# Performance work log

Hardware: AMD Instinct MI355X
Metric: run time of the kernel (lower is better)

Reference implementation:

```python
import jax, jax.numpy as jnp
import numpy as np

N = 100000; E = 1600000; D_IN = 9; HID = 16; HEADS = 8; D = HID * HEADS; G = 1000
NEG_SLOPE = 0.2; LN_EPS = 1e-5


def _gat_conv(x, src, dst, W, a_src, a_dst, b, heads, ch):
    # PyG GATConv (eval mode, self-loops already appended to src/dst)
    h = (x @ W).reshape(-1, heads, ch)                   # [N,H,C]
    al_s = (h * a_src).sum(-1)                           # [N,H]
    al_d = (h * a_dst).sum(-1)                           # [N,H]
    e = al_s[src] + al_d[dst]                            # [Et,H]
    e = jnp.where(e > 0, e, NEG_SLOPE * e)               # LeakyReLU(0.2)
    m = jax.ops.segment_max(e, dst, num_segments=N)      # per-dst softmax
    alpha = jnp.exp(e - m[dst])
    denom = jax.ops.segment_sum(alpha, dst, num_segments=N)
    alpha = alpha / (denom[dst] + 1e-16)
    out = jax.ops.segment_sum(h[src] * alpha[:, :, None], dst, num_segments=N)
    return out.reshape(-1, heads * ch) + b


def _ln_graph(x, g, b):
    # PyG LayerNorm, mode='graph', batch=None: normalize over all nodes+channels
    mu = x.mean()
    var = jnp.mean((x - mu) ** 2)
    return (x - mu) / jnp.sqrt(var + LN_EPS) * g + b


def setup_inputs() -> dict:
    key = jax.random.key(0)
    ks = jax.random.split(key, 20)
    s = 0.1
    p = lambda i, shape: jax.random.normal(ks[i], shape, jnp.float32) * s
    return {
        "x": jax.random.normal(ks[0], (N, D_IN), jnp.float32),
        "edge_index": jax.random.randint(ks[1], (2, E), 0, N),
        "batch": jnp.sort(jax.random.randint(ks[2], (N,), 0, G)),
        "W1": p(3, (D_IN, D)), "a_src1": p(4, (HEADS, HID)), "a_dst1": p(5, (HEADS, HID)), "b1": jnp.zeros((D,), jnp.float32),
        "W2": p(6, (D, D)), "a_src2": p(7, (1, D)), "a_dst2": p(8, (1, D)), "b2": jnp.zeros((D,), jnp.float32),
        "fc1_w": p(9, (D, D)), "fc1_b": jnp.zeros((D,), jnp.float32),
        "fc2_w": p(10, (D, D)), "fc2_b": jnp.zeros((D,), jnp.float32),
        "fc3_w": p(11, (D, D)), "fc3_b": jnp.zeros((D,), jnp.float32),
        "fc4_w": p(12, (D, D)), "fc4_b": jnp.zeros((D,), jnp.float32),
        "g1": jnp.ones((D,), jnp.float32), "beta1": jnp.zeros((D,), jnp.float32),
        "g2": jnp.ones((D,), jnp.float32), "beta2": jnp.zeros((D,), jnp.float32),
        "fcf_w": p(13, (D, 1)), "fcf_b": jnp.zeros((1,), jnp.float32),
    }


def reference(x, edge_index, batch, W1, a_src1, a_dst1, b1, W2, a_src2, a_dst2, b2,
              fc1_w, fc1_b, fc2_w, fc2_b, fc3_w, fc3_b, fc4_w, fc4_b,
              g1, beta1, g2, beta2, fcf_w, fcf_b):
    loops = jnp.arange(N)
    src = jnp.concatenate([edge_index[0], loops])
    dst = jnp.concatenate([edge_index[1], loops])
    h = jax.nn.relu(_gat_conv(x, src, dst, W1, a_src1, a_dst1, b1, HEADS, HID))
    hc = h
    h = jax.nn.relu(h @ fc1_w + fc1_b)
    h = jax.nn.relu(h @ fc2_w + fc2_b + hc)
    h = _ln_graph(h, g1, beta1)
    hc = h
    h = _gat_conv(h, src, dst, W2, a_src2, a_dst2, b2, 1, D)
    h = jax.nn.relu(h @ fc3_w + fc3_b)
    h = h @ fc4_w + fc4_b + hc
    h = _ln_graph(h, g2, beta2)
    h = h @ fcf_w + fcf_b                                # [N,1]
    sums = jax.ops.segment_sum(h, batch, num_segments=G)
    cnt = jax.ops.segment_sum(jnp.ones((N,), h.dtype), batch, num_segments=G)
    return sums / jnp.maximum(cnt, 1.0)[:, None]          # global_mean_pool -> [G,1]
```

## Files before the change

kernel.cpp:

```cpp
#include <hip/hip_runtime.h>
#include <cstdint>

#define NN 100000
#define NE 1600000
#define DI 9
#define DD 128
#define NH 8
#define NG 1000

#define NBK 3125
#define NBLK 256
#define EPB (NE/NBLK)

typedef unsigned int uint;
typedef __attribute__((ext_vector_type(8))) short bf16x8;
typedef __attribute__((ext_vector_type(4))) float f32x4;

__device__ __forceinline__ float leaky(float x){ return x > 0.f ? x : 0.2f*x; }
__device__ __forceinline__ uint f2bf(float f){
  uint u = __float_as_uint(f);
  return (u + 0x7fffu + ((u>>16)&1u)) >> 16;
}
__device__ __forceinline__ float bflo(uint p){ return __uint_as_float(p << 16); }
__device__ __forceinline__ float bfhi(uint p){ return __uint_as_float(p & 0xffff0000u); }
__device__ __forceinline__ uint packbf(float a, float b){ return f2bf(a) | (f2bf(b)<<16); }

union U16 { uint4 u; bf16x8 v; };
__device__ __forceinline__ bf16x8 ld8(const uint* p){ U16 t; t.u = *(const uint4*)p; return t.v; }

__global__ __launch_bounds__(512) void k_hist(const int* __restrict__ dst, int* __restrict__ hist){
  __shared__ int h[NBK];
  for (int i = threadIdx.x; i < NBK; i += 512) h[i] = 0;
  __syncthreads();
  int blk = blockIdx.x;
  int beg = blk*EPB, end = beg + EPB;
  for (int i = beg + threadIdx.x; i < end; i += 512)
    atomicAdd(&h[dst[i] >> 5], 1);
  __syncthreads();
  for (int b = threadIdx.x; b < NBK; b += 512) hist[(size_t)blk*NBK + b] = h[b];
}

__global__ __launch_bounds__(256) void k_bsum(int* __restrict__ hist, int* __restrict__ bsum){
  int b = blockIdx.x*256 + threadIdx.x;
  if (b >= NBK) return;
  int run = 0;
  for (int k = 0; k < NBLK; ++k){
    int t = hist[(size_t)k*NBK + b];
    hist[(size_t)k*NBK + b] = run;
    run += t;
  }
  bsum[b] = run;
}

__global__ __launch_bounds__(1024) void k_bscan(const int* __restrict__ bsum, int* __restrict__ bbase){
  __shared__ int sh[1024];
  __shared__ int carry;
  if (threadIdx.x == 0) carry = 0;
  __syncthreads();
  for (int c0 = 0; c0 < NBK; c0 += 1024){
    int i = c0 + threadIdx.x;
    int v = (i < NBK) ? bsum[i] : 0;
    sh[threadIdx.x] = v;
    __syncthreads();
    for (int off = 1; off < 1024; off <<= 1){
      int t = (threadIdx.x >= off) ? sh[threadIdx.x-off] : 0;
      __syncthreads();
      sh[threadIdx.x] += t;
      __syncthreads();
    }
    if (i < NBK) bbase[i] = carry + sh[threadIdx.x] - v;
    __syncthreads();
    if (threadIdx.x == 0) carry += sh[1023];
    __syncthreads();
  }
}

__global__ __launch_bounds__(512) void k_part(const int* __restrict__ src, const int* __restrict__ dst,
    const int* __restrict__ hist, const int* __restrict__ bbase, uint* __restrict__ ebuf){
  __shared__ int cur[NBK];
  int blk = blockIdx.x;
  for (int b = threadIdx.x; b < NBK; b += 512)
    cur[b] = hist[(size_t)blk*NBK + b] + bbase[b];
  __syncthreads();
  int beg = blk*EPB, end = beg + EPB;
  for (int i = beg + threadIdx.x; i < end; i += 512){
    int d = dst[i], s = src[i];
    int b = d >> 5;
    int p = atomicAdd(&cur[b], 1);
    ebuf[p] = (uint)s | ((uint)(d & 31) << 26);
  }
}

__global__ __launch_bounds__(64) void k_fin(const uint* __restrict__ ebuf, const int* __restrict__ bbase,
    const int* __restrict__ bsum, int* __restrict__ rowptr, int* __restrict__ col){
  __shared__ int cnt32[32];
  __shared__ int exc[32];
  int b = blockIdx.x;
  int lane = threadIdx.x;
  if (lane < 32) cnt32[lane] = 0;
  __syncthreads();
  int base = bbase[b], n = bsum[b];
  for (int i = lane; i < n; i += 64)
    atomicAdd(&cnt32[ebuf[base+i] >> 26], 1);
  __syncthreads();
  if (lane == 0){
    int run = 0;
    for (int d = 0; d < 32; ++d){
      int t = cnt32[d];
      exc[d] = run;
      rowptr[b*32 + d] = base + run;
      run += t;
    }
  }
  __syncthreads();
  if (lane < 32) cnt32[lane] = exc[lane];
  __syncthreads();
  for (int i = lane; i < n; i += 64){
    uint e = ebuf[base+i];
    int d = e >> 26;
    int r = atomicAdd(&cnt32[d], 1);
    col[base + r] = (int)(e & 0x03ffffffu);
  }
  if (b == 0 && lane == 0) rowptr[NN] = NE;
}

__global__ __launch_bounds__(64) void k_wconv(const float* __restrict__ W, uint* __restrict__ WT){
  int n = blockIdx.x;
  int t = threadIdx.x;
  float w0 = W[(2*t)*DD + n];
  float w1 = W[(2*t+1)*DD + n];
  WT[n*64 + t] = packbf(w0, w1);
}

__global__ __launch_bounds__(128) void k_lin1(const float* __restrict__ x, const float* __restrict__ W1,
    const float* __restrict__ as1, const float* __restrict__ ad1,
    uint* __restrict__ t1b, float* __restrict__ al_s, float* __restrict__ al_d){
  int n = blockIdx.x;
  int c = threadIdx.x;
  const float* xr = x + n*DI;
  float t = 0.f;
  #pragma unroll
  for (int k = 0; k < DI; ++k) t = fmaf(xr[k], W1[k*DD+c], t);
  uint mybf = f2bf(t);
  uint pbf  = (uint)__shfl_xor((int)mybf, 1, 64);
  if (!(c & 1)) t1b[(size_t)n*64 + (c>>1)] = mybf | (pbf<<16);
  float vs = t * as1[c];
  float vd = t * ad1[c];
  #pragma unroll
  for (int m = 8; m >= 1; m >>= 1){ vs += __shfl_xor(vs, m, 16); vd += __shfl_xor(vd, m, 16); }
  if ((c & 15) == 0){
    al_s[n*NH + (c>>4)] = vs;
    al_d[n*NH + (c>>4)] = vd;
  }
}

__global__ __launch_bounds__(256) void k_attn1(const float* __restrict__ al_s, const float* __restrict__ al_d,
    const int* __restrict__ rowptr, const int* __restrict__ col,
    float* __restrict__ alpha, float* __restrict__ a0n, float* __restrict__ invden){
  int n = blockIdx.x*4 + (threadIdx.x >> 6);
  if (n >= NN) return;
  int lane = threadIdx.x & 63;
  int h = lane & 7, j = lane >> 3;
  int beg = rowptr[n], end = rowptr[n+1];
  float ald = al_d[n*NH + h];
  float es = leaky(al_s[n*NH + h] + ald);
  float vmax = -3.4e38f;
  for (int e = beg + j; e < end; e += 8){
    int s = col[e];
    vmax = fmaxf(vmax, leaky(al_s[s*NH + h] + ald));
  }
  vmax = fmaxf(vmax, __shfl_xor(vmax, 8, 64));
  vmax = fmaxf(vmax, __shfl_xor(vmax, 16, 64));
  vmax = fmaxf(vmax, __shfl_xor(vmax, 32, 64));
  float m = fmaxf(es, vmax);
  float sl = 0.f;
  for (int e = beg + j; e < end; e += 8){
    int s = col[e];
    float a = __expf(leaky(al_s[s*NH + h] + ald) - m);
    alpha[(size_t)e*NH + h] = a;
    sl += a;
  }
  sl += __shfl_xor(sl, 8, 64);
  sl += __shfl_xor(sl, 16, 64);
  sl += __shfl_xor(sl, 32, 64);
  float a0 = __expf(es - m);
  float inv = 1.f/(a0 + sl + 1e-16f);
  if (j == 0){
    a0n[n*NH + h]    = a0*inv;
    invden[n*NH + h] = inv;
  }
}

__global__ __launch_bounds__(256) void k_gat1g(const uint* __restrict__ t1b,
    const float* __restrict__ alpha, const float* __restrict__ a0n, const float* __restrict__ invden,
    const int* __restrict__ rowptr, const int* __restrict__ col,
    const float* __restrict__ b1, uint* __restrict__ outb){
  int n = blockIdx.x*4 + (threadIdx.x >> 6);
  if (n >= NN) return;
  int lane = threadIdx.x & 63;
  int h = lane >> 3;
  int beg = rowptr[n], end = rowptr[n+1];
  float s0 = 0.f, s1 = 0.f;
  int e = beg;
  for (; e + 4 <= end; e += 4){
    int c0 = col[e], c1 = col[e+1], c2 = col[e+2], c3 = col[e+3];
    float a0_ = alpha[(size_t)e*NH + h];
    float a1_ = alpha[(size_t)(e+1)*NH + h];
    float a2_ = alpha[(size_t)(e+2)*NH + h];
    float a3_ = alpha[(size_t)(e+3)*NH + h];
    uint p0 = t1b[(size_t)c0*64 + lane];
    uint p1 = t1b[(size_t)c1*64 + lane];
    uint p2 = t1b[(size_t)c2*64 + lane];
    uint p3 = t1b[(size_t)c3*64 + lane];
    s0 = fmaf(a0_, bflo(p0), s0); s1 = fmaf(a0_, bfhi(p0), s1);
    s0 = fmaf(a1_, bflo(p1), s0); s1 = fmaf(a1_, bfhi(p1), s1);
    s0 = fmaf(a2_, bflo(p2), s0); s1 = fmaf(a2_, bfhi(p2), s1);
    s0 = fmaf(a3_, bflo(p3), s0); s1 = fmaf(a3_, bfhi(p3), s1);
  }
  for (; e < end; ++e){
    float a = alpha[(size_t)e*NH + h];
    uint p = t1b[(size_t)col[e]*64 + lane];
    s0 = fmaf(a, bflo(p), s0); s1 = fmaf(a, bfhi(p), s1);
  }
  uint ps = t1b[(size_t)n*64 + lane];
  float inv = invden[n*NH + h], az = a0n[n*NH + h];
  float2 bb = ((const float2*)b1)[lane];
  float r0 = fmaf(inv, s0, az*bflo(ps)) + bb.x;
  float r1 = fmaf(inv, s1, az*bfhi(ps)) + bb.y;
  outb[(size_t)n*64 + lane] = packbf(fmaxf(r0,0.f), fmaxf(r1,0.f));
}

__global__ __launch_bounds__(256) void k_al2(const uint* __restrict__ t2b,
    const float* __restrict__ as2, const float* __restrict__ ad2,
    float* __restrict__ al_s, float* __restrict__ al_d){
  int n = blockIdx.x*4 + (threadIdx.x >> 6);
  if (n >= NN) return;
  int lane = threadIdx.x & 63;
  uint p = t2b[(size_t)n*64 + lane];
  float v0 = bflo(p), v1 = bfhi(p);
  float2 s2 = ((const float2*)as2)[lane];
  float2 d2 = ((const float2*)ad2)[lane];
  float vs = v0*s2.x + v1*s2.y;
  float vd = v0*d2.x + v1*d2.y;
  #pragma unroll
  for (int m = 32; m >= 1; m >>= 1){ vs += __shfl_xor(vs, m, 64); vd += __shfl_xor(vd, m, 64); }
  if (lane == 0){ al_s[n] = vs; al_d[n] = vd; }
}

__global__ __launch_bounds__(256) void k_attn2(const float* __restrict__ al_s, const float* __restrict__ al_d,
    const int* __restrict__ rowptr, const int* __restrict__ col,
    float* __restrict__ alpha, float* __restrict__ a0n, float* __restrict__ invden){
  int n = blockIdx.x*4 + (threadIdx.x >> 6);
  if (n >= NN) return;
  int lane = threadIdx.x & 63;
  int beg = rowptr[n], end = rowptr[n+1];
  float ald = al_d[n];
  float es = leaky(al_s[n] + ald);
  float vmax = -3.4e38f;
  for (int e = beg + lane; e < end; e += 64)
    vmax = fmaxf(vmax, leaky(al_s[col[e]] + ald));
  #pragma unroll
  for (int mk = 32; mk >= 1; mk >>= 1) vmax = fmaxf(vmax, __shfl_xor(vmax, mk, 64));
  float m = fmaxf(es, vmax);
  float sl = 0.f;
  for (int e = beg + lane; e < end; e += 64){
    float a = __expf(leaky(al_s[col[e]] + ald) - m);
    alpha[e] = a;
    sl += a;
  }
  #pragma unroll
  for (int mk = 32; mk >= 1; mk >>= 1) sl += __shfl_xor(sl, mk, 64);
  float a0 = __expf(es - m);
  float inv = 1.f/(a0 + sl + 1e-16f);
  if (lane == 0){ a0n[n] = a0*inv; invden[n] = inv; }
}

__global__ __launch_bounds__(256) void k_gat2g(const uint* __restrict__ t2b,
    const float* __restrict__ alpha, const float* __restrict__ a0n, const float* __restrict__ invden,
    const int* __restrict__ rowptr, const int* __restrict__ col,
    const float* __restrict__ b2, uint* __restrict__ outb){
  int n = blockIdx.x*4 + (threadIdx.x >> 6);
  if (n >= NN) return;
  int lane = threadIdx.x & 63;
  int beg = rowptr[n], end = rowptr[n+1];
  float s0 = 0.f, s1 = 0.f;
  int e = beg;
  for (; e + 4 <= end; e += 4){
    int c0 = col[e], c1 = col[e+1], c2 = col[e+2], c3 = col[e+3];
    float a0_ = alpha[e],   a1_ = alpha[e+1];
    float a2_ = alpha[e+2], a3_ = alpha[e+3];
    uint p0 = t2b[(size_t)c0*64 + lane];
    uint p1 = t2b[(size_t)c1*64 + lane];
    uint p2 = t2b[(size_t)c2*64 + lane];
    uint p3 = t2b[(size_t)c3*64 + lane];
    s0 = fmaf(a0_, bflo(p0), s0); s1 = fmaf(a0_, bfhi(p0), s1);
    s0 = fmaf(a1_, bflo(p1), s0); s1 = fmaf(a1_, bfhi(p1), s1);
    s0 = fmaf(a2_, bflo(p2), s0); s1 = fmaf(a2_, bfhi(p2), s1);
    s0 = fmaf(a3_, bflo(p3), s0); s1 = fmaf(a3_, bfhi(p3), s1);
  }
  for (; e < end; ++e){
    float a = alpha[e];
    uint p = t2b[(size_t)col[e]*64 + lane];
    s0 = fmaf(a, bflo(p), s0); s1 = fmaf(a, bfhi(p), s1);
  }
  uint ps = t2b[(size_t)n*64 + lane];
  float inv = invden[n], az = a0n[n];
  float2 bb = ((const float2*)b2)[lane];
  float r0 = fmaf(inv, s0, az*bflo(ps)) + bb.x;
  float r1 = fmaf(inv, s1, az*bfhi(ps)) + bb.y;
  outb[(size_t)n*64 + lane] = packbf(r0, r1);
}

template<bool RELU, bool BIAS, bool RES>
__global__ __launch_bounds__(256) void k_mfma(const uint* __restrict__ Xb, const uint* __restrict__ WTb,
    const float* __restrict__ bias, const uint* __restrict__ resb, uint* __restrict__ outb, int nrows){
  int lane = threadIdx.x & 63;
  int wid  = threadIdx.x >> 6;
  int m0 = blockIdx.x*128 + wid*32;
  int lr = lane & 15, hi4 = lane >> 4;
  f32x4 acc[2][8];
  #pragma unroll
  for (int a = 0; a < 2; ++a)
    #pragma unroll
    for (int c = 0; c < 8; ++c) acc[a][c] = (f32x4){0.f,0.f,0.f,0.f};
  int ra0 = m0 + lr;      if (ra0 > NN-1) ra0 = NN-1;
  int ra1 = m0 + 16 + lr; if (ra1 > NN-1) ra1 = NN-1;
  #pragma unroll
  for (int kk = 0; kk < 4; ++kk){
    int ko = kk*16 + hi4*4;
    bf16x8 a0 = ld8(Xb + (size_t)ra0*64 + ko);
    bf16x8 a1 = ld8(Xb + (size_t)ra1*64 + ko);
    #pragma unroll
    for (int c = 0; c < 8; ++c){
      bf16x8 b = ld8(WTb + (size_t)(c*16 + lr)*64 + ko);
      acc[0][c] = __builtin_amdgcn_mfma_f32_16x16x32_bf16(a0, b, acc[0][c], 0, 0, 0);
      acc[1][c] = __builtin_amdgcn_mfma_f32_16x16x32_bf16(a1, b, acc[1][c], 0, 0, 0);
    }
  }
  bool evn = !(lane & 1);
  int cph = lr >> 1;
  #pragma unroll
  for (int rg = 0; rg < 2; ++rg){
    #pragma unroll
    for (int c = 0; c < 8; ++c){
      int cp = c*8 + cph;
      #pragma unroll
      for (int r = 0; r < 4; ++r){
        float v0 = acc[rg][c][r];
        float v1 = __shfl_xor(v0, 1, 64);
        int row = m0 + rg*16 + hi4*4 + r;
        if (evn && row < nrows){
          if (BIAS){ float2 bb = ((const float2*)bias)[cp]; v0 += bb.x; v1 += bb.y; }
          if (RES){ uint rr = resb[(size_t)row*64 + cp]; v0 += bflo(rr); v1 += bfhi(rr); }
          if (RELU){ v0 = fmaxf(v0, 0.f); v1 = fmaxf(v1, 0.f); }
          outb[(size_t)row*64 + cp] = packbf(v0, v1);
        }
      }
    }
  }
}

__global__ __launch_bounds__(256) void k_ln_reduce_bf(const uint* __restrict__ xb, float* __restrict__ pbuf){
  const uint4* x4 = (const uint4*)xb;
  const int n4 = NN*16;
  float s = 0.f, ss = 0.f;
  for (int i = blockIdx.x*256 + threadIdx.x; i < n4; i += gridDim.x*256){
    uint4 u = x4[i];
    float a, b;
    a = bflo(u.x); b = bfhi(u.x); s += a+b; ss += a*a + b*b;
    a = bflo(u.y); b = bfhi(u.y); s += a+b; ss += a*a + b*b;
    a = bflo(u.z); b = bfhi(u.z); s += a+b; ss += a*a + b*b;
    a = bflo(u.w); b = bfhi(u.w); s += a+b; ss += a*a + b*b;
  }
  #pragma unroll
  for (int m = 32; m >= 1; m >>= 1){ s += __shfl_xor(s, m, 64); ss += __shfl_xor(ss, m, 64); }
  __shared__ float sh[8];
  int wid = threadIdx.x >> 6, lane = threadIdx.x & 63;
  if (lane == 0){ sh[wid*2] = s; sh[wid*2+1] = ss; }
  __syncthreads();
  if (threadIdx.x == 0){
    float S = 0.f, SS = 0.f;
    for (int w = 0; w < 4; ++w){ S += sh[2*w]; SS += sh[2*w+1]; }
    pbuf[blockIdx.x*2] = S; pbuf[blockIdx.x*2+1] = SS;
  }
}

__global__ __launch_bounds__(256) void k_ln_stats(const float* __restrict__ pbuf, float* __restrict__ stats, int nb){
  float s = 0.f, ss = 0.f;
  for (int i = threadIdx.x; i < nb; i += 256){ s += pbuf[2*i]; ss += pbuf[2*i+1]; }
  #pragma unroll
  for (int m = 32; m >= 1; m >>= 1){ s += __shfl_xor(s, m, 64); ss += __shfl_xor(ss, m, 64); }
  __shared__ float sh[8];
  int wid = threadIdx.x >> 6, lane = threadIdx.x & 63;
  if (lane == 0){ sh[wid*2] = s; sh[wid*2+1] = ss; }
  __syncthreads();
  if (threadIdx.x == 0){
    float S = 0.f, SS = 0.f;
    for (int w = 0; w < 4; ++w){ S += sh[2*w]; SS += sh[2*w+1]; }
    const float inv = 1.f/((float)NN*(float)DD);
    float mu = S*inv;
    float var = SS*inv - mu*mu;
    stats[0] = mu;
    stats[1] = rsqrtf(var + 1e-5f);
  }
}

__global__ __launch_bounds__(256) void k_ln_apply_bf(uint* __restrict__ xb, const float* __restrict__ g,
    const float* __restrict__ be, const float* __restrict__ stats){
  const int n4 = NN*16;
  float mu = stats[0], rs = stats[1];
  uint4* x4 = (uint4*)xb;
  const float2* g2 = (const float2*)g;
  const float2* b2 = (const float2*)be;
  for (int i = blockIdx.x*256 + threadIdx.x; i < n4; i += gridDim.x*256){
    int cb = (i & 15)*4;
    uint4 u = x4[i];
    float2 ga = g2[cb],   gb = g2[cb+1], gc = g2[cb+2], gd = g2[cb+3];
    float2 ba = b2[cb],   bb = b2[cb+1], bc = b2[cb+2], bd = b2[cb+3];
    u.x = packbf((bflo(u.x)-mu)*rs*ga.x + ba.x, (bfhi(u.x)-mu)*rs*ga.y + ba.y);
    u.y = packbf((bflo(u.y)-mu)*rs*gb.x + bb.x, (bfhi(u.y)-mu)*rs*gb.y + bb.y);
    u.z = packbf((bflo(u.z)-mu)*rs*gc.x + bc.x, (bfhi(u.z)-mu)*rs*gc.y + bc.y);
    u.w = packbf((bflo(u.w)-mu)*rs*gd.x + bd.x, (bfhi(u.w)-mu)*rs*gd.y + bd.y);
    x4[i] = u;
  }
}

__global__ __launch_bounds__(256) void k_fdot_ln(const uint* __restrict__ xb, const float* __restrict__ g,
    const float* __restrict__ be, const float* __restrict__ stats,
    const float* __restrict__ fw, const float* __restrict__ fb, float* __restrict__ val){
  int n = blockIdx.x*4 + (threadIdx.x >> 6);
  if (n >= NN) return;
  int lane = threadIdx.x & 63;
  float mu = stats[0], rs = stats[1];
  uint p = xb[(size_t)n*64 + lane];
  float2 gg = ((const float2*)g)[lane];
  float2 bb = ((const float2*)be)[lane];
  float2 ww = ((const float2*)fw)[lane];
  float v = ((bflo(p)-mu)*rs*gg.x + bb.x)*ww.x + ((bfhi(p)-mu)*rs*gg.y + bb.y)*ww.y;
  #pragma unroll
  for (int m = 32; m >= 1; m >>= 1) v += __shfl_xor(v, m, 64);
  if (lane == 0) val[n] = v + fb[0];
}

__global__ __launch_bounds__(64) void k_pool(const float* __restrict__ val, const int* __restrict__ batch,
                                             float* __restrict__ out){
  int g = blockIdx.x;
  int lane = threadIdx.x;
  int lo = 0, hi = NN;
  while (lo < hi){ int mid = (lo+hi)>>1; if (batch[mid] < g) lo = mid+1; else hi = mid; }
  int start = lo;
  hi = NN;
  while (lo < hi){ int mid = (lo+hi)>>1; if (batch[mid] < g+1) lo = mid+1; else hi = mid; }
  int end = lo;
  float s = 0.f;
  for (int i = start + lane; i < end; i += 64) s += val[i];
  #pragma unroll
  for (int m = 32; m >= 1; m >>= 1) s += __shfl_xor(s, m, 64);
  if (lane == 0) out[g] = s / fmaxf((float)(end - start), 1.f);
}

extern "C" void kernel_launch(void* const* d_in, const int* in_sizes, int n_in,
                              void* d_out, int out_size, void* d_ws, size_t ws_size,
                              hipStream_t stream){
  const float* x   = (const float*)d_in[0];
  const int*   ei  = (const int*)d_in[1];
  const int* batch = (const int*)d_in[2];
  const float* W1  = (const float*)d_in[3];
  const float* as1 = (const float*)d_in[4];
  const float* ad1 = (const float*)d_in[5];
  const float* b1  = (const float*)d_in[6];
  const float* W2  = (const float*)d_in[7];
  const float* as2 = (const float*)d_in[8];
  const float* ad2 = (const float*)d_in[9];
  const float* b2  = (const float*)d_in[10];
  const float* fc1w= (const float*)d_in[11];
  const float* fc1b= (const float*)d_in[12];
  const float* fc2w= (const float*)d_in[13];
  const float* fc2b= (const float*)d_in[14];
  const float* fc3w= (const float*)d_in[15];
  const float* fc3b= (const float*)d_in[16];
  const float* fc4w= (const float*)d_in[17];
  const float* fc4b= (const float*)d_in[18];
  const float* g1  = (const float*)d_in[19];
  const float* be1 = (const float*)d_in[20];
  const float* g2  = (const float*)d_in[21];
  const float* be2 = (const float*)d_in[22];
  const float* fcw = (const float*)d_in[23];
  const float* fcb = (const float*)d_in[24];
  float* out = (float*)d_out;
  (void)in_sizes; (void)n_in; (void)out_size; (void)ws_size;

  char* ws = (char*)d_ws;
  size_t off = 0;
  auto alloc = [&](size_t bytes)->void*{
    void* p = ws + off;
    off += (bytes + 255) & ~(size_t)255;
    return p;
  };
  float* A    = (float*)alloc((size_t)NN*DD*4);
  float* B    = (float*)alloc((size_t)NN*DD*4);
  float* C    = (float*)alloc((size_t)NN*DD*4);
  float* als1 = (float*)alloc((size_t)NN*NH*4);
  float* ald1 = (float*)alloc((size_t)NN*NH*4);
  float* a0n1 = (float*)alloc((size_t)NN*NH*4);
  float* inv1 = (float*)alloc((size_t)NN*NH*4);
  float* als2 = (float*)alloc((size_t)NN*4);
  float* ald2 = (float*)alloc((size_t)NN*4);
  float* a0n2 = (float*)alloc((size_t)NN*4);
  float* inv2 = (float*)alloc((size_t)NN*4);
  float* alpha2 = (float*)alloc((size_t)NE*4);
  int*   rowptr = (int*)alloc((size_t)(NN+1)*4);
  int*   col    = (int*)alloc((size_t)NE*4);
  int*   bsum   = (int*)alloc((size_t)NBK*4);
  int*   bbase  = (int*)alloc((size_t)NBK*4);
  float* pbuf   = (float*)alloc(1024*2*4);
  float* stats  = (float*)alloc(2*4);
  float* val    = (float*)alloc((size_t)NN*4);
  uint* wt_fc1  = (uint*)alloc((size_t)DD*64*4);
  uint* wt_fc2  = (uint*)alloc((size_t)DD*64*4);
  uint* wt_w2   = (uint*)alloc((size_t)DD*64*4);
  uint* wt_fc3  = (uint*)alloc((size_t)DD*64*4);
  uint* wt_fc4  = (uint*)alloc((size_t)DD*64*4);

  float* alpha1 = C;
  uint*  Ab     = (uint*)A;
  uint*  Bb     = (uint*)B;
  uint*  Cb     = (uint*)C;
  int*   hist   = (int*)A;
  uint*  ebuf   = (uint*)alpha2;

  const int* esrc = ei;
  const int* edst = ei + NE;

  k_hist <<<NBLK, 512, 0, stream>>>(edst, hist);
  k_bsum <<<(NBK+255)/256, 256, 0, stream>>>(hist, bsum);
  k_bscan<<<1, 1024, 0, stream>>>(bsum, bbase);
  k_part <<<NBLK, 512, 0, stream>>>(esrc, edst, hist, bbase, ebuf);
  k_fin  <<<NBK, 64, 0, stream>>>(ebuf, bbase, bsum, rowptr, col);

  k_wconv<<<DD, 64, 0, stream>>>(fc1w, wt_fc1);
  k_wconv<<<DD, 64, 0, stream>>>(fc2w, wt_fc2);
  k_wconv<<<DD, 64, 0, stream>>>(W2,   wt_w2);
  k_wconv<<<DD, 64, 0, stream>>>(fc3w, wt_fc3);
  k_wconv<<<DD, 64, 0, stream>>>(fc4w, wt_fc4);

  const int WB = (NN + 3)/4;
  const int GB = (NN + 127)/128;

  k_lin1<<<NN, 128, 0, stream>>>(x, W1, as1, ad1, Ab, als1, ald1);
  k_attn1<<<WB, 256, 0, stream>>>(als1, ald1, rowptr, col, alpha1, a0n1, inv1);
  k_gat1g<<<WB, 256, 0, stream>>>(Ab, alpha1, a0n1, inv1, rowptr, col, b1, Bb);

  k_mfma<true,  true, false><<<GB, 256, 0, stream>>>(Bb, wt_fc1, fc1b, nullptr, Ab, NN);
  k_mfma<true,  true, true ><<<GB, 256, 0, stream>>>(Ab, wt_fc2, fc2b, Bb,      Cb, NN);

  k_ln_reduce_bf<<<1024, 256, 0, stream>>>(Cb, pbuf);
  k_ln_stats<<<1, 256, 0, stream>>>(pbuf, stats, 1024);
  k_ln_apply_bf<<<1024, 256, 0, stream>>>(Cb, g1, be1, stats);

  k_mfma<false, false, false><<<GB, 256, 0, stream>>>(Cb, wt_w2, nullptr, nullptr, Ab, NN);
  k_al2<<<WB, 256, 0, stream>>>(Ab, as2, ad2, als2, ald2);
  k_attn2<<<WB, 256, 0, stream>>>(als2, ald2, rowptr, col, alpha2, a0n2, inv2);
  k_gat2g<<<WB, 256, 0, stream>>>(Ab, alpha2, a0n2, inv2, rowptr, col, b2, Bb);

  k_mfma<true,  true, false><<<GB, 256, 0, stream>>>(Bb, wt_fc3, fc3b, nullptr, Ab, NN);
  k_mfma<false, true, true ><<<GB, 256, 0, stream>>>(Ab, wt_fc4, fc4b, Cb,      Bb, NN);

  k_ln_reduce_bf<<<1024, 256, 0, stream>>>(Bb, pbuf);
  k_ln_stats<<<1, 256, 0, stream>>>(pbuf, stats, 1024);
  k_fdot_ln<<<WB, 256, 0, stream>>>(Bb, g2, be2, stats, fcw, fcb, val);
  k_pool<<<NG, 64, 0, stream>>>(val, batch, out);
}
```

Baseline: 561.3 us.

## Fuse GAT softmax into aggregation and fold LayerNorm reduction into MFMA epilogue

Removes the separate attention kernels. Each aggregation kernel now computes the unnormalized exp weights on the fly, without max subtraction, and divides by the accumulated denominator at the end. This avoids writing and re-reading the per-edge alpha arrays and launching extra kernels. The LayerNorm sum and sum-of-squares reduction is moved into the epilogue of the residual MFMA GEMM, so the separate full read pass over the activations goes away. Dropping the max subtraction risks overflow in exp for large logits, and the LN statistics are now summed from fp32 values before bf16 rounding.

```diff
diff --git a/kernel.cpp b/kernel.cpp
--- a/kernel.cpp
+++ b/kernel.cpp
@@ -154,80 +154,49 @@
   }
 }
 
-__global__ __launch_bounds__(256) void k_attn1(const float* __restrict__ al_s, const float* __restrict__ al_d,
-    const int* __restrict__ rowptr, const int* __restrict__ col,
-    float* __restrict__ alpha, float* __restrict__ a0n, float* __restrict__ invden){
-  int n = blockIdx.x*4 + (threadIdx.x >> 6);
-  if (n >= NN) return;
-  int lane = threadIdx.x & 63;
-  int h = lane & 7, j = lane >> 3;
-  int beg = rowptr[n], end = rowptr[n+1];
-  float ald = al_d[n*NH + h];
-  float es = leaky(al_s[n*NH + h] + ald);
-  float vmax = -3.4e38f;
-  for (int e = beg + j; e < end; e += 8){
-    int s = col[e];
-    vmax = fmaxf(vmax, leaky(al_s[s*NH + h] + ald));
-  }
-  vmax = fmaxf(vmax, __shfl_xor(vmax, 8, 64));
-  vmax = fmaxf(vmax, __shfl_xor(vmax, 16, 64));
-  vmax = fmaxf(vmax, __shfl_xor(vmax, 32, 64));
-  float m = fmaxf(es, vmax);
-  float sl = 0.f;
-  for (int e = beg + j; e < end; e += 8){
-    int s = col[e];
-    float a = __expf(leaky(al_s[s*NH + h] + ald) - m);
-    alpha[(size_t)e*NH + h] = a;
-    sl += a;
-  }
-  sl += __shfl_xor(sl, 8, 64);
-  sl += __shfl_xor(sl, 16, 64);
-  sl += __shfl_xor(sl, 32, 64);
-  float a0 = __expf(es - m);
-  float inv = 1.f/(a0 + sl + 1e-16f);
-  if (j == 0){
-    a0n[n*NH + h]    = a0*inv;
-    invden[n*NH + h] = inv;
-  }
-}
-
-__global__ __launch_bounds__(256) void k_gat1g(const uint* __restrict__ t1b,
-    const float* __restrict__ alpha, const float* __restrict__ a0n, const float* __restrict__ invden,
+__global__ __launch_bounds__(256) void k_gat1(const uint* __restrict__ t1b,
+    const float* __restrict__ al_s, const float* __restrict__ al_d,
     const int* __restrict__ rowptr, const int* __restrict__ col,
     const float* __restrict__ b1, uint* __restrict__ outb){
   int n = blockIdx.x*4 + (threadIdx.x >> 6);
   if (n >= NN) return;
-  int lane = threadIdx.x & 63;
-  int h = lane >> 3;
+  uint lane = threadIdx.x & 63;
+  uint h = lane >> 3;
+  float ald = al_d[(uint)n*NH + h];
+  float a0  = __expf(leaky(al_s[(uint)n*NH + h] + ald));
+  uint  ps  = t1b[(uint)n*64u + lane];
+  float den = a0;
+  float s0 = a0*bflo(ps), s1 = a0*bfhi(ps);
   int beg = rowptr[n], end = rowptr[n+1];
-  float s0 = 0.f, s1 = 0.f;
   int e = beg;
   for (; e + 4 <= end; e += 4){
-    int c0 = col[e], c1 = col[e+1], c2 = col[e+2], c3 = col[e+3];
-    float a0_ = alpha[(size_t)e*NH + h];
-    float a1_ = alpha[(size_t)(e+1)*NH + h];
-    float a2_ = alpha[(size_t)(e+2)*NH + h];
-    float a3_ = alpha[(size_t)(e+3)*NH + h];
-    uint p0 = t1b[(size_t)c0*64 + lane];
-    uint p1 = t1b[(size_t)c1*64 + lane];
-    uint p2 = t1b[(size_t)c2*64 + lane];
-    uint p3 = t1b[(size_t)c3*64 + lane];
+    uint c0 = (uint)col[e], c1 = (uint)col[e+1], c2 = (uint)col[e+2], c3 = (uint)col[e+3];
+    float l0 = al_s[c0*8u + h], l1 = al_s[c1*8u + h];
+    float l2 = al_s[c2*8u + h], l3 = al_s[c3*8u + h];
+    uint p0 = t1b[c0*64u + lane];
+    uint p1 = t1b[c1*64u + lane];
+    uint p2 = t1b[c2*64u + lane];
+    uint p3 = t1b[c3*64u + lane];
+    float a0_ = __expf(leaky(l0 + ald));
+    float a1_ = __expf(leaky(l1 + ald));
+    float a2_ = __expf(leaky(l2 + ald));
+    float a3_ = __expf(leaky(l3 + ald));
+    den += a0_ + a1_ + a2_ + a3_;
     s0 = fmaf(a0_, bflo(p0), s0); s1 = fmaf(a0_, bfhi(p0), s1);
     s0 = fmaf(a1_, bflo(p1), s0); s1 = fmaf(a1_, bfhi(p1), s1);
     s0 = fmaf(a2_, bflo(p2), s0); s1 = fmaf(a2_, bfhi(p2), s1);
     s0 = fmaf(a3_, bflo(p3), s0); s1 = fmaf(a3_, bfhi(p3), s1);
   }
   for (; e < end; ++e){
-    float a = alpha[(size_t)e*NH + h];
-    uint p = t1b[(size_t)col[e]*64 + lane];
+    uint c = (uint)col[e];
+    float a = __expf(leaky(al_s[c*8u + h] + ald));
+    uint p = t1b[c*64u + lane];
+    den += a;
     s0 = fmaf(a, bflo(p), s0); s1 = fmaf(a, bfhi(p), s1);
   }
-  uint ps = t1b[(size_t)n*64 + lane];
-  float inv = invden[n*NH + h], az = a0n[n*NH + h];
+  float inv = 1.f/(den + 1e-16f);
   float2 bb = ((const float2*)b1)[lane];
-  float r0 = fmaf(inv, s0, az*bflo(ps)) + bb.x;
-  float r1 = fmaf(inv, s1, az*bfhi(ps)) + bb.y;
-  outb[(size_t)n*64 + lane] = packbf(fmaxf(r0,0.f), fmaxf(r1,0.f));
+  outb[(uint)n*64u + lane] = packbf(fmaxf(s0*inv + bb.x, 0.f), fmaxf(s1*inv + bb.y, 0.f));
 }
 
 __global__ __launch_bounds__(256) void k_al2(const uint* __restrict__ t2b,
@@ -247,73 +216,53 @@
   if (lane == 0){ al_s[n] = vs; al_d[n] = vd; }
 }
 
-__global__ __launch_bounds__(256) void k_attn2(const float* __restrict__ al_s, const float* __restrict__ al_d,
-    const int* __restrict__ rowptr, const int* __restrict__ col,
-    float* __restrict__ alpha, float* __restrict__ a0n, float* __restrict__ invden){
-  int n = blockIdx.x*4 + (threadIdx.x >> 6);
-  if (n >= NN) return;
-  int lane = threadIdx.x & 63;
-  int beg = rowptr[n], end = rowptr[n+1];
-  float ald = al_d[n];
-  float es = leaky(al_s[n] + ald);
-  float vmax = -3.4e38f;
-  for (int e = beg + lane; e < end; e += 64)
-    vmax = fmaxf(vmax, leaky(al_s[col[e]] + ald));
-  #pragma unroll
-  for (int mk = 32; mk >= 1; mk >>= 1) vmax = fmaxf(vmax, __shfl_xor(vmax, mk, 64));
-  float m = fmaxf(es, vmax);
-  float sl = 0.f;
-  for (int e = beg + lane; e < end; e += 64){
-    float a = __expf(leaky(al_s[col[e]] + ald) - m);
-    alpha[e] = a;
-    sl += a;
-  }
-  #pragma unroll
-  for (int mk = 32; mk >= 1; mk >>= 1) sl += __shfl_xor(sl, mk, 64);
-  float a0 = __expf(es - m);
-  float inv = 1.f/(a0 + sl + 1e-16f);
-  if (lane == 0){ a0n[n] = a0*inv; invden[n] = inv; }
-}
-
-__global__ __launch_bounds__(256) void k_gat2g(const uint* __restrict__ t2b,
-    const float* __restrict__ alpha, const float* __restrict__ a0n, const float* __restrict__ invden,
+__global__ __launch_bounds__(256) void k_gat2(const uint* __restrict__ t2b,
+    const float* __restrict__ al_s, const float* __restrict__ al_d,
     const int* __restrict__ rowptr, const int* __restrict__ col,
     const float* __restrict__ b2, uint* __restrict__ outb){
   int n = blockIdx.x*4 + (threadIdx.x >> 6);
   if (n >= NN) return;
-  int lane = threadIdx.x & 63;
+  uint lane = threadIdx.x & 63;
+  float ald = al_d[n];
+  float a0  = __expf(leaky(al_s[n] + ald));
+  uint  ps  = t2b[(uint)n*64u + lane];
+  float den = a0;
+  float s0 = a0*bflo(ps), s1 = a0*bfhi(ps);
   int beg = rowptr[n], end = rowptr[n+1];
-  float s0 = 0.f, s1 = 0.f;
   int e = beg;
   for (; e + 4 <= end; e += 4){
-    int c0 = col[e], c1 = col[e+1], c2 = col[e+2], c3 = col[e+3];
-    float a0_ = alpha[e],   a1_ = alpha[e+1];
-    float a2_ = alpha[e+2], a3_ = alpha[e+3];
-    uint p0 = t2b[(size_t)c0*64 + lane];
-    uint p1 = t2b[(size_t)c1*64 + lane];
-    uint p2 = t2b[(size_t)c2*64 + lane];
-    uint p3 = t2b[(size_t)c3*64 + lane];
+    uint c0 = (uint)col[e], c1 = (uint)col[e+1], c2 = (uint)col[e+2], c3 = (uint)col[e+3];
+    float l0 = al_s[c0], l1 = al_s[c1], l2 = al_s[c2], l3 = al_s[c3];
+    uint p0 = t2b[c0*64u + lane];
+    uint p1 = t2b[c1*64u + lane];
+    uint p2 = t2b[c2*64u + lane];
+    uint p3 = t2b[c3*64u + lane];
+    float a0_ = __expf(leaky(l0 + ald));
+    float a1_ = __expf(leaky(l1 + ald));
+    float a2_ = __expf(leaky(l2 + ald));
+    float a3_ = __expf(leaky(l3 + ald));
+    den += a0_ + a1_ + a2_ + a3_;
     s0 = fmaf(a0_, bflo(p0), s0); s1 = fmaf(a0_, bfhi(p0), s1);
     s0 = fmaf(a1_, bflo(p1), s0); s1 = fmaf(a1_, bfhi(p1), s1);
     s0 = fmaf(a2_, bflo(p2), s0); s1 = fmaf(a2_, bfhi(p2), s1);
     s0 = fmaf(a3_, bflo(p3), s0); s1 = fmaf(a3_, bfhi(p3), s1);
   }
   for (; e < end; ++e){
-    float a = alpha[e];
-    uint p = t2b[(size_t)col[e]*64 + lane];
+    uint c = (uint)col[e];
+    float a = __expf(leaky(al_s[c] + ald));
+    uint p = t2b[c*64u + lane];
+    den += a;
     s0 = fmaf(a, bflo(p), s0); s1 = fmaf(a, bfhi(p), s1);
   }
-  uint ps = t2b[(size_t)n*64 + lane];
-  float inv = invden[n], az = a0n[n];
+  float inv = 1.f/(den + 1e-16f);
   float2 bb = ((const float2*)b2)[lane];
-  float r0 = fmaf(inv, s0, az*bflo(ps)) + bb.x;
-  float r1 = fmaf(inv, s1, az*bfhi(ps)) + bb.y;
-  outb[(size_t)n*64 + lane] = packbf(r0, r1);
-}
-
-template<bool RELU, bool BIAS, bool RES>
+  outb[(uint)n*64u + lane] = packbf(s0*inv + bb.x, s1*inv + bb.y);
+}
+
+template<bool RELU, bool BIAS, bool RES, bool LNRED>
 __global__ __launch_bounds__(256) void k_mfma(const uint* __restrict__ Xb, const uint* __restrict__ WTb,
-    const float* __restrict__ bias, const uint* __restrict__ resb, uint* __restrict__ outb, int nrows){
+    const float* __restrict__ bias, const uint* __restrict__ resb, uint* __restrict__ outb,
+    float* __restrict__ pbuf, int nrows){
   int lane = threadIdx.x & 63;
   int wid  = threadIdx.x >> 6;
   int m0 = blockIdx.x*128 + wid*32;
@@ -339,6 +288,7 @@
   }
   bool evn = !(lane & 1);
   int cph = lr >> 1;
+  float lns = 0.f, lnss = 0.f;
   #pragma unroll
   for (int rg = 0; rg < 2; ++rg){
     #pragma unroll
@@ -354,34 +304,22 @@
           if (RES){ uint rr = resb[(size_t)row*64 + cp]; v0 += bflo(rr); v1 += bfhi(rr); }
           if (RELU){ v0 = fmaxf(v0, 0.f); v1 = fmaxf(v1, 0.f); }
           outb[(size_t)row*64 + cp] = packbf(v0, v1);
+          if (LNRED){ lns += v0 + v1; lnss += v0*v0 + v1*v1; }
         }
       }
     }
   }
-}
-
-__global__ __launch_bounds__(256) void k_ln_reduce_bf(const uint* __restrict__ xb, float* __restrict__ pbuf){
-  const uint4* x4 = (const uint4*)xb;
-  const int n4 = NN*16;
-  float s = 0.f, ss = 0.f;
-  for (int i = blockIdx.x*256 + threadIdx.x; i < n4; i += gridDim.x*256){
-    uint4 u = x4[i];
-    float a, b;
-    a = bflo(u.x); b = bfhi(u.x); s += a+b; ss += a*a + b*b;
-    a = bflo(u.y); b = bfhi(u.y); s += a+b; ss += a*a + b*b;
-    a = bflo(u.z); b = bfhi(u.z); s += a+b; ss += a*a + b*b;
-    a = bflo(u.w); b = bfhi(u.w); s += a+b; ss += a*a + b*b;
-  }
-  #pragma unroll
-  for (int m = 32; m >= 1; m >>= 1){ s += __shfl_xor(s, m, 64); ss += __shfl_xor(ss, m, 64); }
-  __shared__ float sh[8];
-  int wid = threadIdx.x >> 6, lane = threadIdx.x & 63;
-  if (lane == 0){ sh[wid*2] = s; sh[wid*2+1] = ss; }
-  __syncthreads();
-  if (threadIdx.x == 0){
-    float S = 0.f, SS = 0.f;
-    for (int w = 0; w < 4; ++w){ S += sh[2*w]; SS += sh[2*w+1]; }
-    pbuf[blockIdx.x*2] = S; pbuf[blockIdx.x*2+1] = SS;
+  if (LNRED){
+    #pragma unroll
+    for (int m = 32; m >= 1; m >>= 1){ lns += __shfl_xor(lns, m, 64); lnss += __shfl_xor(lnss, m, 64); }
+    __shared__ float shred[8];
+    if (lane == 0){ shred[wid*2] = lns; shred[wid*2+1] = lnss; }
+    __syncthreads();
+    if (threadIdx.x == 0){
+      float S = 0.f, SS = 0.f;
+      for (int w = 0; w < 4; ++w){ S += shred[2*w]; SS += shred[2*w+1]; }
+      pbuf[blockIdx.x*2] = S; pbuf[blockIdx.x*2+1] = SS;
+    }
   }
 }
 
@@ -502,13 +440,9 @@
   float* C    = (float*)alloc((size_t)NN*DD*4);
   float* als1 = (float*)alloc((size_t)NN*NH*4);
   float* ald1 = (float*)alloc((size_t)NN*NH*4);
-  float* a0n1 = (float*)alloc((size_t)NN*NH*4);
-  float* inv1 = (float*)alloc((size_t)NN*NH*4);
   float* als2 = (float*)alloc((size_t)NN*4);
   float* ald2 = (float*)alloc((size_t)NN*4);
-  float* a0n2 = (float*)alloc((size_t)NN*4);
-  float* inv2 = (float*)alloc((size_t)NN*4);
-  float* alpha2 = (float*)alloc((size_t)NE*4);
+  float* escr = (float*)alloc((size_t)NE*4);
   int*   rowptr = (int*)alloc((size_t)(NN+1)*4);
   int*   col    = (int*)alloc((size_t)NE*4);
   int*   bsum   = (int*)alloc((size_t)NBK*4);
@@ -522,12 +456,11 @@
   uint* wt_fc3  = (uint*)alloc((size_t)DD*64*4);
   uint* wt_fc4  = (uint*)alloc((size_t)DD*64*4);
 
-  float* alpha1 = C;
   uint*  Ab     = (uint*)A;
   uint*  Bb     = (uint*)B;
   uint*  Cb     = (uint*)C;
   int*   hist   = (int*)A;
-  uint*  ebuf   = (uint*)alpha2;
+  uint*  ebuf   = (uint*)escr;
 
   const int* esrc = ei;
   const int* edst = ei + NE;
@@ -548,26 +481,22 @@
   const int GB = (NN + 127)/128;
 
   k_lin1<<<NN, 128, 0, stream>>>(x, W1, as1, ad1, Ab, als1, ald1);
-  k_attn1<<<WB, 256, 0, stream>>>(als1, ald1, rowptr, col, alpha1, a0n1, inv1);
-  k_gat1g<<<WB, 256, 0, stream>>>(Ab, alpha1, a0n1, inv1, rowptr, col, b1, Bb);
-
-  k_mfma<true,  true, false><<<GB, 256, 0, stream>>>(Bb, wt_fc1, fc1b, nullptr, Ab, NN);
-  k_mfma<true,  true, true ><<<GB, 256, 0, stream>>>(Ab, wt_fc2, fc2b, Bb,      Cb, NN);
-
-  k_ln_reduce_bf<<<1024, 256, 0, stream>>>(Cb, pbuf);
-  k_ln_stats<<<1, 256, 0, stream>>>(pbuf, stats, 1024);
+  k_gat1<<<WB, 256, 0, stream>>>(Ab, als1, ald1, rowptr, col, b1, Bb);
+
+  k_mfma<true,  true, false, false><<<GB, 256, 0, stream>>>(Bb, wt_fc1, fc1b, nullptr, Ab, nullptr, NN);
+  k_mfma<true,  true, true,  true ><<<GB, 256, 0, stream>>>(Ab, wt_fc2, fc2b, Bb,      Cb, pbuf,    NN);
+
+  k_ln_stats<<<1, 256, 0, stream>>>(pbuf, stats, GB);
   k_ln_apply_bf<<<1024, 256, 0, stream>>>(Cb, g1, be1, stats);
 
-  k_mfma<false, false, false><<<GB, 256, 0, stream>>>(Cb, wt_w2, nullptr, nullptr, Ab, NN);
+  k_mfma<false, false, false, false><<<GB, 256, 0, stream>>>(Cb, wt_w2, nullptr, nullptr, Ab, nullptr, NN);
   k_al2<<<WB, 256, 0, stream>>>(Ab, as2, ad2, als2, ald2);
-  k_attn2<<<WB, 256, 0, stream>>>(als2, ald2, rowptr, col, alpha2, a0n2, inv2);
-  k_gat2g<<<WB, 256, 0, stream>>>(Ab, alpha2, a0n2, inv2, rowptr, col, b2, Bb);
-
-  k_mfma<true,  true, false><<<GB, 256, 0, stream>>>(Bb, wt_fc3, fc3b, nullptr, Ab, NN);
-  k_mfma<false, true, true ><<<GB, 256, 0, stream>>>(Ab, wt_fc4, fc4b, Cb,      Bb, NN);
-
-  k_ln_reduce_bf<<<1024, 256, 0, stream>>>(Bb, pbuf);
-  k_ln_stats<<<1, 256, 0, stream>>>(pbuf, stats, 1024);
+  k_gat2<<<WB, 256, 0, stream>>>(Ab, als2, ald2, rowptr, col, b2, Bb);
+
+  k_mfma<true,  true, false, false><<<GB, 256, 0, stream>>>(Bb, wt_fc3, fc3b, nullptr, Ab, nullptr, NN);
+  k_mfma<false, true, true,  true ><<<GB, 256, 0, stream>>>(Ab, wt_fc4, fc4b, Cb,      Bb, pbuf,    NN);
+
+  k_ln_stats<<<1, 256, 0, stream>>>(pbuf, stats, GB);
   k_fdot_ln<<<WB, 256, 0, stream>>>(Bb, g2, be2, stats, fcw, fcb, val);
   k_pool<<<NG, 64, 0, stream>>>(val, batch, out);
 }
```

Result: faster. 484.0 us (-13.8%).
